# Kernel optimization log

Hardware: AMD Instinct MI355X
Metric: run time of the kernel (lower is better)

Reference implementation:

```python
import jax, jax.numpy as jnp
import numpy as np

DIM = 64
HEADS = 8
DIM_HEAD = 64
INNER = HEADS * DIM_HEAD  # 512
FB, HB, WB = 3, 4, 4
Q_L = HB * WB            # 16
KV_L = FB * HB * WB      # 48
EPS = 1e-5


def conv3(x, W):
    # x: [N,Cin,H,W], W: [Cout,Cin,3,3], stride 1, pad 1, no bias
    return jax.lax.conv_general_dilated(
        x, W, window_strides=(1, 1), padding='SAME',
        dimension_numbers=('NCHW', 'OIHW', 'NCHW'))


def layernorm(x, g, b):
    # normalize over last (channel) dim, matching nn.LayerNorm(dim)
    mu = jnp.mean(x, axis=-1, keepdims=True)
    var = jnp.mean(jnp.square(x - mu), axis=-1, keepdims=True)
    return (x - mu) * jax.lax.rsqrt(var + EPS) * g + b


def warp_nearest(x, flow):
    # Faithful to flow_warp-style grid_sample(mode='nearest', padding='zeros',
    # align_corners=True): sample x at round(grid + flow), zeros out-of-range.
    n, c, h, w = x.shape
    gy, gx = jnp.meshgrid(jnp.arange(h, dtype=x.dtype),
                          jnp.arange(w, dtype=x.dtype), indexing='ij')
    px = gx[None] + flow[:, 0]  # [n,h,w]
    py = gy[None] + flow[:, 1]
    ix = jnp.round(px).astype(jnp.int32)
    iy = jnp.round(py).astype(jnp.int32)
    valid = (ix >= 0) & (ix < w) & (iy >= 0) & (iy < h)
    flat = jnp.clip(iy, 0, h - 1) * w + jnp.clip(ix, 0, w - 1)  # [n,h,w]

    def gather_one(xi, fi):
        return jnp.take(xi.reshape(c, h * w), fi.reshape(-1), axis=1).reshape(c, h, w)

    out = jax.vmap(gather_one)(x, flat)
    return out * valid[:, None].astype(x.dtype)


def setup_inputs() -> dict:
    key = jax.random.key(0)
    ks = jax.random.split(key, 12)
    b, h, w = 2, 128, 128
    inp = {
        'q_inp': jax.random.normal(ks[0], (b, 1, DIM, h, w), jnp.float32),
        'k_inp': jax.random.normal(ks[1], (b, 3, DIM, h, w), jnp.float32),
        'flow_f': jax.random.normal(ks[2], (b, 2, h, w), jnp.float32) * 4.0,
        'flow_b': jax.random.normal(ks[3], (b, 2, h, w), jnp.float32) * 4.0,
        'gq': jnp.ones((DIM,), jnp.float32),
        'bq': jnp.zeros((DIM,), jnp.float32),
        'gkv': jnp.ones((DIM,), jnp.float32),
        'bkv': jnp.zeros((DIM,), jnp.float32),
        'Wq': jax.random.normal(ks[4], (INNER, DIM, 3, 3), jnp.float32) * 0.02,
        'Wkv': jax.random.normal(ks[5], (2 * INNER, DIM, 3, 3), jnp.float32) * 0.02,
        'Wout': jax.random.normal(ks[6], (DIM, INNER, 3, 3), jnp.float32) * 0.02,
        'static_a': jax.random.truncated_normal(ks[7], -2.0, 2.0, (1, HEADS, Q_L, KV_L), jnp.float32),
    }
    return inp


def _fgsw_msa(q_inp, k_inp, flow_f, flow_b, gq, bq, gkv, bkv, Wq, Wkv, Wout, static_a):
    b, f_q, c, h, w = q_inp.shape
    # flow-guided warp of forward/backward key frames (nearest, zeros padding)
    k_f = warp_nearest(k_inp[:, 0], flow_f)
    k_r = k_inp[:, 1]
    k_b = warp_nearest(k_inp[:, 2], flow_b)
    k_stack = jnp.stack([k_f, k_r, k_b], axis=1)  # [b,3,c,h,w]

    # LayerNorm over channels
    qn = layernorm(q_inp.transpose(0, 1, 3, 4, 2), gq, bq).transpose(0, 1, 4, 2, 3)
    kvn = layernorm(k_stack.transpose(0, 1, 3, 4, 2), gkv, bkv).transpose(0, 1, 4, 2, 3)

    # conv QKV projections
    q = conv3(qn.reshape(b * f_q, c, h, w), Wq)       # [b, INNER, h, w]
    kv = conv3(kvn.reshape(b * 3, c, h, w), Wkv)      # [3b, 2*INNER, h, w]
    k, v = jnp.split(kv, 2, axis=1)

    nh, nw = h // HB, w // WB

    def part(t, f):
        # [(b f), C, H, W] -> [(b nh nw), heads, f*HB*WB, d]
        C = t.shape[1]
        t = t.reshape(b, f, C, nh, HB, nw, WB)
        t = t.transpose(0, 3, 5, 1, 4, 6, 2)  # b, nh, nw, f, p1, p2, C
        t = t.reshape(b * nh * nw, f * HB * WB, HEADS, C // HEADS)
        return t.transpose(0, 2, 1, 3)

    qh = part(q, f_q) * (DIM_HEAD ** -0.5)
    kh = part(k, 3)
    vh = part(v, 3)

    sim = jnp.einsum('bhid,bhjd->bhij', qh, kh) + static_a
    attn = jax.nn.softmax(sim, axis=-1)
    out = jnp.einsum('bhij,bhjd->bhid', attn, vh)  # [(b nh nw), heads, Q_L, d]

    out = out.transpose(0, 2, 1, 3).reshape(b * nh * nw, f_q * HB * WB, INNER)
    out = out.reshape(b, nh, nw, f_q, HB, WB, INNER)
    out = out.transpose(0, 3, 6, 1, 4, 2, 5).reshape(b * f_q, INNER, h, w)
    out = conv3(out, Wout).reshape(b, f_q, c, h, w)
    return out


def reference(q_inp, k_inp, flow_f, flow_b, gq, bq, gkv, bkv, Wq, Wkv, Wout, static_a):
    return _fgsw_msa(q_inp, k_inp, flow_f, flow_b, gq, bq, gkv, bkv, Wq, Wkv, Wout, static_a)
```

## Files before the change

### kernel.cpp

```cpp
#include <hip/hip_runtime.h>


typedef __attribute__((ext_vector_type(8))) short bf16x8;
typedef __attribute__((ext_vector_type(4))) float f32x4;

__device__ __forceinline__ float bs2f(unsigned short s) {
    return __uint_as_float(((unsigned int)s) << 16);
}
__device__ __forceinline__ unsigned short f2bs(float f) {
    unsigned int u = __float_as_uint(f);
    u += 0x7fffu + ((u >> 16) & 1u);
    return (unsigned short)(u >> 16);
}

__global__ __launch_bounds__(256) void ln_q_kernel(
    const float* __restrict__ q_inp, const float* __restrict__ g,
    const float* __restrict__ b, unsigned short* __restrict__ qn)
{
    int wid  = (blockIdx.x * 256 + threadIdx.x) >> 6;
    int lane = threadIdx.x & 63;
    int pix  = wid & 16383;
    int bb   = wid >> 14;
    float val = q_inp[(bb * 64 + lane) * 16384 + pix];
    float s = val;
    #pragma unroll
    for (int m = 1; m < 64; m <<= 1) s += __shfl_xor(s, m);
    float mu = s * (1.f / 64.f);
    float d = val - mu;
    float s2 = d * d;
    #pragma unroll
    for (int m = 1; m < 64; m <<= 1) s2 += __shfl_xor(s2, m);
    float o = d * rsqrtf(s2 * (1.f / 64.f) + 1e-5f) * g[lane] + b[lane];
    qn[wid * 64 + lane] = f2bs(o);
}

__global__ __launch_bounds__(256) void warp_ln_kv_kernel(
    const float* __restrict__ k_inp, const float* __restrict__ flow_f,
    const float* __restrict__ flow_b, const float* __restrict__ g,
    const float* __restrict__ b, unsigned short* __restrict__ kvn)
{
    int wid  = (blockIdx.x * 256 + threadIdx.x) >> 6;
    int lane = threadIdx.x & 63;
    int x  = wid & 127;
    int y  = (wid >> 7) & 127;
    int bf = wid >> 14;
    int f  = bf % 3, bb = bf / 3;
    float val;
    if (f == 1) {
        val = k_inp[(bf * 64 + lane) * 16384 + y * 128 + x];
    } else {
        const float* fl = (f == 0) ? flow_f : flow_b;
        float fx = fl[(bb * 2 + 0) * 16384 + y * 128 + x];
        float fy = fl[(bb * 2 + 1) * 16384 + y * 128 + x];
        int ix = (int)rintf((float)x + fx);
        int iy = (int)rintf((float)y + fy);
        if (ix >= 0 && ix < 128 && iy >= 0 && iy < 128)
            val = k_inp[(bf * 64 + lane) * 16384 + iy * 128 + ix];
        else
            val = 0.f;
    }
    float s = val;
    #pragma unroll
    for (int m = 1; m < 64; m <<= 1) s += __shfl_xor(s, m);
    float mu = s * (1.f / 64.f);
    float d = val - mu;
    float s2 = d * d;
    #pragma unroll
    for (int m = 1; m < 64; m <<= 1) s2 += __shfl_xor(s2, m);
    float o = d * rsqrtf(s2 * (1.f / 64.f) + 1e-5f) * g[lane] + b[lane];
    kvn[wid * 64 + lane] = f2bs(o);
}

__global__ __launch_bounds__(256) void repack_bf16_kernel(
    const float* __restrict__ w, unsigned short* __restrict__ wp,
    int IC, int total)
{
    int idx = blockIdx.x * 256 + threadIdx.x;
    if (idx >= total) return;
    int tap = idx % 9;
    int tmp = idx / 9;
    int ic  = tmp % IC;
    int oc  = tmp / IC;
    wp[oc * IC * 9 + (ic >> 6) * 576 + tap * 64 + (ic & 63)] = f2bs(w[idx]);
}

__global__ __launch_bounds__(256) void fused_attn_kernel(
    const unsigned short* __restrict__ qn,
    const unsigned short* __restrict__ kvn,
    const unsigned short* __restrict__ wq,
    const unsigned short* __restrict__ wkv,
    const float* __restrict__ sa,
    unsigned short* __restrict__ ao)
{
    __shared__ __align__(16) unsigned char smem[49088];
    unsigned short* kvp = (unsigned short*)smem;
    unsigned short* qls = (unsigned short*)(smem + 15552);
    unsigned short* kls = (unsigned short*)(smem + 32192);
    unsigned short* vls = (unsigned short*)(smem + 39104);
    float*          atl = (float*)(smem + 46016);
    unsigned short* qpatch = kls;

    const int tid  = threadIdx.x;
    const int lane = tid & 63;
    const int w    = tid >> 6;
    const int wx = blockIdx.x & 31, wy = blockIdx.x >> 5;
    const int bb = blockIdx.y;
    const int gx0 = wx * 4 - 1, gy0 = wy * 4 - 1;

    for (int u = tid; u < 864; u += 256) {
        int f = u / 288, rest = u - f * 288;
        int pos = rest >> 3, seg = rest & 7;
        int hy = pos / 6, hx = pos - hy * 6;
        int gy = gy0 + hy, gx = gx0 + hx;
        uint4 v = make_uint4(0u, 0u, 0u, 0u);
        if ((unsigned)gy < 128u && (unsigned)gx < 128u)
            v = *reinterpret_cast<const uint4*>(
                kvn + (((bb * 3 + f) * 128 + gy) * 128 + gx) * 64 + seg * 8);
        *reinterpret_cast<uint4*>(kvp + (f * 36 + pos) * 72 + seg * 8) = v;
    }
    for (int u = tid; u < 288; u += 256) {
        int pos = u >> 3, seg = u & 7;
        int hy = pos / 6, hx = pos - hy * 6;
        int gy = gy0 + hy, gx = gx0 + hx;
        uint4 v = make_uint4(0u, 0u, 0u, 0u);
        if ((unsigned)gy < 128u && (unsigned)gx < 128u)
            v = *reinterpret_cast<const uint4*>(
                qn + ((bb * 128 + gy) * 128 + gx) * 64 + seg * 8);
        *reinterpret_cast<uint4*>(qpatch + pos * 72 + seg * 8) = v;
    }
    __syncthreads();

    const int r  = lane & 15;
    const int kg = lane >> 4;
    const int py = r >> 2, px = r & 3;

    for (int g = 0; g < 2; ++g) {
        f32x4 acc0 = {0.f,0.f,0.f,0.f}, acc1 = acc0, acc2 = acc0, acc3 = acc0;
        #pragma unroll 3
        for (int kk = 0; kk < 18; ++kk) {
            int tap = kk >> 1, ic0 = (kk & 1) * 32;
            int ky = tap / 3, kx = tap - ky * 3;
            int pos = (py + ky) * 6 + (px + kx);
            bf16x8 a = *reinterpret_cast<const bf16x8*>(qpatch + pos * 72 + ic0 + kg * 8);
            const unsigned short* wb = wq + (w * 8 + g * 4) * 16 * 576 + kk * 32 + kg * 8;
            bf16x8 b0 = *reinterpret_cast<const bf16x8*>(wb + (0 * 16 + r) * 576);
            bf16x8 b1 = *reinterpret_cast<const bf16x8*>(wb + (1 * 16 + r) * 576);
            bf16x8 b2 = *reinterpret_cast<const bf16x8*>(wb + (2 * 16 + r) * 576);
            bf16x8 b3 = *reinterpret_cast<const bf16x8*>(wb + (3 * 16 + r) * 576);
            acc0 = __builtin_amdgcn_mfma_f32_16x16x32_bf16(a, b0, acc0, 0, 0, 0);
            acc1 = __builtin_amdgcn_mfma_f32_16x16x32_bf16(a, b1, acc1, 0, 0, 0);
            acc2 = __builtin_amdgcn_mfma_f32_16x16x32_bf16(a, b2, acc2, 0, 0, 0);
            acc3 = __builtin_amdgcn_mfma_f32_16x16x32_bf16(a, b3, acc3, 0, 0, 0);
        }
        #pragma unroll
        for (int reg = 0; reg < 4; ++reg) {
            int row = kg * 4 + reg;
            int cb  = (w * 8 + g * 4) * 16 + r;
            qls[row * 520 + cb +  0] = f2bs(0.125f * acc0[reg]);
            qls[row * 520 + cb + 16] = f2bs(0.125f * acc1[reg]);
            qls[row * 520 + cb + 32] = f2bs(0.125f * acc2[reg]);
            qls[row * 520 + cb + 48] = f2bs(0.125f * acc3[reg]);
        }
    }
    __syncthreads();

    const int is_v = w >> 1, pair = w & 1;
    const int qi = tid >> 4, qjg = tid & 15;
    const int pd = tid & 63, pig = tid >> 6;

    for (int h = 0; h < 8; ++h) {
        {
            f32x4 c00 = {0.f,0.f,0.f,0.f}, c01 = c00, c10 = c00, c11 = c00, c20 = c00, c21 = c00;
            #pragma unroll 3
            for (int kk = 0; kk < 18; ++kk) {
                int tap = kk >> 1, ic0 = (kk & 1) * 32;
                int ky = tap / 3, kx = tap - ky * 3;
                int pos = (py + ky) * 6 + (px + kx);
                bf16x8 a0 = *reinterpret_cast<const bf16x8*>(kvp + pos * 72 + ic0 + kg * 8);
                bf16x8 a1 = *reinterpret_cast<const bf16x8*>(kvp + (36 + pos) * 72 + ic0 + kg * 8);
                bf16x8 a2 = *reinterpret_cast<const bf16x8*>(kvp + (72 + pos) * 72 + ic0 + kg * 8);
                int ocb = is_v * 512 + h * 64 + pair * 32;
                const unsigned short* wb = wkv + (size_t)ocb * 576 + kk * 32 + kg * 8;
                bf16x8 b0 = *reinterpret_cast<const bf16x8*>(wb + (size_t)(r) * 576);
                bf16x8 b1 = *reinterpret_cast<const bf16x8*>(wb + (size_t)(16 + r) * 576);
                c00 = __builtin_amdgcn_mfma_f32_16x16x32_bf16(a0, b0, c00, 0, 0, 0);
                c10 = __builtin_amdgcn_mfma_f32_16x16x32_bf16(a1, b0, c10, 0, 0, 0);
                c20 = __builtin_amdgcn_mfma_f32_16x16x32_bf16(a2, b0, c20, 0, 0, 0);
                c01 = __builtin_amdgcn_mfma_f32_16x16x32_bf16(a0, b1, c01, 0, 0, 0);
                c11 = __builtin_amdgcn_mfma_f32_16x16x32_bf16(a1, b1, c11, 0, 0, 0);
                c21 = __builtin_amdgcn_mfma_f32_16x16x32_bf16(a2, b1, c21, 0, 0, 0);
            }
            unsigned short* dst = is_v ? vls : kls;
            #pragma unroll
            for (int reg = 0; reg < 4; ++reg) {
                int jr = kg * 4 + reg;
                int cb = pair * 32 + r;
                dst[(jr +  0) * 72 + cb]      = f2bs(c00[reg]);
                dst[(jr + 16) * 72 + cb]      = f2bs(c10[reg]);
                dst[(jr + 32) * 72 + cb]      = f2bs(c20[reg]);
                dst[(jr +  0) * 72 + cb + 16] = f2bs(c01[reg]);
                dst[(jr + 16) * 72 + cb + 16] = f2bs(c11[reg]);
                dst[(jr + 32) * 72 + cb + 16] = f2bs(c21[reg]);
            }
        }
        __syncthreads();

        {
            const unsigned short* qrow = qls + qi * 520 + h * 64;
            float p[3];
            #pragma unroll
            for (int t = 0; t < 3; ++t) {
                int j = qjg + 16 * t;
                const unsigned short* krow = kls + j * 72;
                float s = 0.f;
                #pragma unroll
                for (int q8 = 0; q8 < 8; ++q8) {
                    uint4 ua = *reinterpret_cast<const uint4*>(qrow + q8 * 8);
                    uint4 ub = *reinterpret_cast<const uint4*>(krow + q8 * 8);
                    const unsigned short* pa = (const unsigned short*)&ua;
                    const unsigned short* pb = (const unsigned short*)&ub;
                    #pragma unroll
                    for (int o = 0; o < 8; ++o) s += bs2f(pa[o]) * bs2f(pb[o]);
                }
                p[t] = s + sa[(h * 16 + qi) * 48 + j];
            }
            float mx = fmaxf(p[0], fmaxf(p[1], p[2]));
            #pragma unroll
            for (int m = 1; m < 16; m <<= 1) mx = fmaxf(mx, __shfl_xor(mx, m));
            float sum = 0.f;
            #pragma unroll
            for (int t = 0; t < 3; ++t) { p[t] = __expf(p[t] - mx); sum += p[t]; }
            #pragma unroll
            for (int m = 1; m < 16; m <<= 1) sum += __shfl_xor(sum, m);
            float inv = 1.f / sum;
            #pragma unroll
            for (int t = 0; t < 3; ++t) atl[qi * 48 + qjg + 16 * t] = p[t] * inv;
        }
        __syncthreads();

        {
            float acc[4] = {0.f, 0.f, 0.f, 0.f};
            for (int j = 0; j < 48; ++j) {
                float vj = bs2f(vls[j * 72 + pd]);
                #pragma unroll
                for (int s = 0; s < 4; ++s)
                    acc[s] += atl[(pig * 4 + s) * 48 + j] * vj;
            }
            #pragma unroll
            for (int s = 0; s < 4; ++s) {
                int ii = pig * 4 + s;
                int y = wy * 4 + (ii >> 2), x = wx * 4 + (ii & 3);
                ao[((bb * 128 + y) * 128 + x) * 512 + h * 64 + pd] = f2bs(acc[s]);
            }
        }
        __syncthreads();
    }
}

__global__ __launch_bounds__(256) void conv512_kernel(
    const unsigned short* __restrict__ in,
    const unsigned short* __restrict__ wp,
    float* __restrict__ out)
{
    __shared__ __align__(16) unsigned short patch[100 * 72];
    const int tid = threadIdx.x, lane = tid & 63, w = tid >> 6;
    const int tx = blockIdx.x & 15, ty = blockIdx.x >> 4;
    const int img = blockIdx.y;
    const int gx0 = tx * 8 - 1, gy0 = ty * 8 - 1;
    const int r = lane & 15, kg = lane >> 4;

    f32x4 acc0 = {0.f,0.f,0.f,0.f}, acc1 = acc0, acc2 = acc0, acc3 = acc0;

    for (int ci = 0; ci < 8; ++ci) {
        __syncthreads();
        for (int u = tid; u < 800; u += 256) {
            int pos = u >> 3, seg = u & 7;
            int hy = pos / 10, hx = pos - hy * 10;
            int gy = gy0 + hy, gx = gx0 + hx;
            uint4 v = make_uint4(0u, 0u, 0u, 0u);
            if ((unsigned)gy < 128u && (unsigned)gx < 128u)
                v = *reinterpret_cast<const uint4*>(
                    in + (((size_t)img * 128 + gy) * 128 + gx) * 512 + ci * 64 + seg * 8);
            *reinterpret_cast<uint4*>(patch + pos * 72 + seg * 8) = v;
        }
        __syncthreads();
        #pragma unroll 3
        for (int kk = 0; kk < 18; ++kk) {
            int tap = kk >> 1, ic0 = (kk & 1) * 32;
            int ky = tap / 3, kx = tap - ky * 3;
            int oc = w * 16 + r;
            bf16x8 b = *reinterpret_cast<const bf16x8*>(
                wp + (size_t)oc * 4608 + ci * 576 + kk * 32 + kg * 8);
            #pragma unroll
            for (int m = 0; m < 4; ++m) {
                int rr = m * 16 + r;
                int pos = ((rr >> 3) + ky) * 10 + (rr & 7) + kx;
                bf16x8 a = *reinterpret_cast<const bf16x8*>(patch + pos * 72 + ic0 + kg * 8);
                f32x4& acc = (m == 0) ? acc0 : (m == 1) ? acc1 : (m == 2) ? acc2 : acc3;
                acc = __builtin_amdgcn_mfma_f32_16x16x32_bf16(a, b, acc, 0, 0, 0);
            }
        }
    }
    const int oc = w * 16 + r;
    #pragma unroll
    for (int m = 0; m < 4; ++m) {
        const f32x4& acc = (m == 0) ? acc0 : (m == 1) ? acc1 : (m == 2) ? acc2 : acc3;
        int r0 = m * 16 + kg * 4;
        int gy = ty * 8 + (r0 >> 3), gx = tx * 8 + (r0 & 7);
        *reinterpret_cast<float4*>(
            out + (((size_t)img * 64 + oc) * 128 + gy) * 128 + gx) =
            make_float4(acc[0], acc[1], acc[2], acc[3]);
    }
}

extern "C" void kernel_launch(void* const* d_in, const int* in_sizes, int n_in,
                              void* d_out, int out_size, void* d_ws, size_t ws_size,
                              hipStream_t stream)
{
    const float* q_inp  = (const float*)d_in[0];
    const float* k_inp  = (const float*)d_in[1];
    const float* flow_f = (const float*)d_in[2];
    const float* flow_b = (const float*)d_in[3];
    const float* gq     = (const float*)d_in[4];
    const float* bq     = (const float*)d_in[5];
    const float* gkv    = (const float*)d_in[6];
    const float* bkv    = (const float*)d_in[7];
    const float* Wq     = (const float*)d_in[8];
    const float* Wkv    = (const float*)d_in[9];
    const float* Wout   = (const float*)d_in[10];
    const float* sa     = (const float*)d_in[11];

    if (ws_size < 55050240u) return;

    char* ws = (char*)d_ws;
    unsigned short* qn   = (unsigned short*)(ws + 0);
    unsigned short* kvn  = (unsigned short*)(ws + 4194304);
    unsigned short* ao   = (unsigned short*)(ws + 16777216);
    unsigned short* wqb  = (unsigned short*)(ws + 50331648);
    unsigned short* wkvb = (unsigned short*)(ws + 50921472);
    unsigned short* wopb = (unsigned short*)(ws + 52101120);

    ln_q_kernel<<<8192, 256, 0, stream>>>(q_inp, gq, bq, qn);
    warp_ln_kv_kernel<<<24576, 256, 0, stream>>>(k_inp, flow_f, flow_b, gkv, bkv, kvn);

    repack_bf16_kernel<<<1152, 256, 0, stream>>>(Wq,   wqb,  64,  294912);
    repack_bf16_kernel<<<2304, 256, 0, stream>>>(Wkv,  wkvb, 64,  589824);
    repack_bf16_kernel<<<1152, 256, 0, stream>>>(Wout, wopb, 512, 294912);

    fused_attn_kernel<<<dim3(1024, 2), 256, 0, stream>>>(qn, kvn, wqb, wkvb, sa, ao);

    conv512_kernel<<<dim3(256, 2), 256, 0, stream>>>(ao, wopb, (float*)d_out);
}
```

Before: 645.2 us.

## Compute attention QK^T and PV with MFMA instead of scalar loops

Replaces the scalar per-thread QK dot products and the PV accumulation loop in the fused attention kernel with 16x16x32 bf16 MFMA instructions. V is now stored transposed in shared memory, and scores/probabilities live in a padded bf16 buffer so K=48 can be zero-padded to 64. Softmax probabilities and pre-softmax scores are rounded to bf16, which costs some precision. The output write pattern changes to 16-channel slices per wave, with less coalescing per store.

After: 606.8 us. 6.0% less time.

```diff
diff --git a/kernel.cpp b/kernel.cpp
--- a/kernel.cpp
+++ b/kernel.cpp
@@ -92,12 +92,12 @@
     const float* __restrict__ sa,
     unsigned short* __restrict__ ao)
 {
-    __shared__ __align__(16) unsigned char smem[49088];
-    unsigned short* kvp = (unsigned short*)smem;
-    unsigned short* qls = (unsigned short*)(smem + 15552);
-    unsigned short* kls = (unsigned short*)(smem + 32192);
-    unsigned short* vls = (unsigned short*)(smem + 39104);
-    float*          atl = (float*)(smem + 46016);
+    __shared__ __align__(16) unsigned char smem[50624];
+    unsigned short* kvp   = (unsigned short*)smem;
+    unsigned short* qls   = (unsigned short*)(smem + 15552);
+    unsigned short* kls   = (unsigned short*)(smem + 32192);
+    unsigned short* vls_T = (unsigned short*)(smem + 39104);
+    unsigned short* pls   = (unsigned short*)(smem + 48320);
     unsigned short* qpatch = kls;
 
     const int tid  = threadIdx.x;
@@ -127,6 +127,14 @@
             v = *reinterpret_cast<const uint4*>(
                 qn + ((bb * 128 + gy) * 128 + gx) * 64 + seg * 8);
         *reinterpret_cast<uint4*>(qpatch + pos * 72 + seg * 8) = v;
+    }
+    for (int u = tid; u < 1024; u += 256) {
+        int row = u >> 4, c = 48 + (u & 15);
+        vls_T[row * 72 + c] = 0;
+    }
+    if (tid < 256) {
+        int row = tid >> 4, c = 48 + (tid & 15);
+        pls[row * 72 + c] = 0;
     }
     __syncthreads();
 
@@ -165,8 +173,7 @@
     __syncthreads();
 
     const int is_v = w >> 1, pair = w & 1;
-    const int qi = tid >> 4, qjg = tid & 15;
-    const int pd = tid & 63, pig = tid >> 6;
+    const int si = tid >> 4, sjg = tid & 15;
 
     for (int h = 0; h < 8; ++h) {
         {
@@ -190,67 +197,86 @@
                 c11 = __builtin_amdgcn_mfma_f32_16x16x32_bf16(a1, b1, c11, 0, 0, 0);
                 c21 = __builtin_amdgcn_mfma_f32_16x16x32_bf16(a2, b1, c21, 0, 0, 0);
             }
-            unsigned short* dst = is_v ? vls : kls;
+            if (!is_v) {
+                #pragma unroll
+                for (int reg = 0; reg < 4; ++reg) {
+                    int jr = kg * 4 + reg;
+                    int cb = pair * 32 + r;
+                    kls[(jr +  0) * 72 + cb]      = f2bs(c00[reg]);
+                    kls[(jr + 16) * 72 + cb]      = f2bs(c10[reg]);
+                    kls[(jr + 32) * 72 + cb]      = f2bs(c20[reg]);
+                    kls[(jr +  0) * 72 + cb + 16] = f2bs(c01[reg]);
+                    kls[(jr + 16) * 72 + cb + 16] = f2bs(c11[reg]);
+                    kls[(jr + 32) * 72 + cb + 16] = f2bs(c21[reg]);
+                }
+            } else {
+                #pragma unroll
+                for (int reg = 0; reg < 4; ++reg) {
+                    int jr = kg * 4 + reg;
+                    int d0 = pair * 32 + r;
+                    vls_T[d0 * 72        + jr]      = f2bs(c00[reg]);
+                    vls_T[d0 * 72        + 16 + jr] = f2bs(c10[reg]);
+                    vls_T[d0 * 72        + 32 + jr] = f2bs(c20[reg]);
+                    vls_T[(d0 + 16) * 72 + jr]      = f2bs(c01[reg]);
+                    vls_T[(d0 + 16) * 72 + 16 + jr] = f2bs(c11[reg]);
+                    vls_T[(d0 + 16) * 72 + 32 + jr] = f2bs(c21[reg]);
+                }
+            }
+        }
+        __syncthreads();
+
+        if (w < 3) {
+            f32x4 s_acc = {0.f, 0.f, 0.f, 0.f};
+            #pragma unroll
+            for (int s = 0; s < 2; ++s) {
+                bf16x8 a = *reinterpret_cast<const bf16x8*>(
+                    qls + r * 520 + h * 64 + s * 32 + kg * 8);
+                bf16x8 b = *reinterpret_cast<const bf16x8*>(
+                    kls + (w * 16 + r) * 72 + s * 32 + kg * 8);
+                s_acc = __builtin_amdgcn_mfma_f32_16x16x32_bf16(a, b, s_acc, 0, 0, 0);
+            }
             #pragma unroll
             for (int reg = 0; reg < 4; ++reg) {
-                int jr = kg * 4 + reg;
-                int cb = pair * 32 + r;
-                dst[(jr +  0) * 72 + cb]      = f2bs(c00[reg]);
-                dst[(jr + 16) * 72 + cb]      = f2bs(c10[reg]);
-                dst[(jr + 32) * 72 + cb]      = f2bs(c20[reg]);
-                dst[(jr +  0) * 72 + cb + 16] = f2bs(c01[reg]);
-                dst[(jr + 16) * 72 + cb + 16] = f2bs(c11[reg]);
-                dst[(jr + 32) * 72 + cb + 16] = f2bs(c21[reg]);
+                int i = kg * 4 + reg, j = w * 16 + r;
+                float val = s_acc[reg] + sa[(h * 16 + i) * 48 + j];
+                pls[i * 72 + j] = f2bs(val);
             }
         }
         __syncthreads();
 
         {
-            const unsigned short* qrow = qls + qi * 520 + h * 64;
-            float p[3];
-            #pragma unroll
-            for (int t = 0; t < 3; ++t) {
-                int j = qjg + 16 * t;
-                const unsigned short* krow = kls + j * 72;
-                float s = 0.f;
-                #pragma unroll
-                for (int q8 = 0; q8 < 8; ++q8) {
-                    uint4 ua = *reinterpret_cast<const uint4*>(qrow + q8 * 8);
-                    uint4 ub = *reinterpret_cast<const uint4*>(krow + q8 * 8);
-                    const unsigned short* pa = (const unsigned short*)&ua;
-                    const unsigned short* pb = (const unsigned short*)&ub;
-                    #pragma unroll
-                    for (int o = 0; o < 8; ++o) s += bs2f(pa[o]) * bs2f(pb[o]);
-                }
-                p[t] = s + sa[(h * 16 + qi) * 48 + j];
-            }
-            float mx = fmaxf(p[0], fmaxf(p[1], p[2]));
+            float p0 = bs2f(pls[si * 72 + sjg]);
+            float p1 = bs2f(pls[si * 72 + sjg + 16]);
+            float p2 = bs2f(pls[si * 72 + sjg + 32]);
+            float mx = fmaxf(p0, fmaxf(p1, p2));
             #pragma unroll
             for (int m = 1; m < 16; m <<= 1) mx = fmaxf(mx, __shfl_xor(mx, m));
-            float sum = 0.f;
-            #pragma unroll
-            for (int t = 0; t < 3; ++t) { p[t] = __expf(p[t] - mx); sum += p[t]; }
+            p0 = __expf(p0 - mx); p1 = __expf(p1 - mx); p2 = __expf(p2 - mx);
+            float sum = p0 + p1 + p2;
             #pragma unroll
             for (int m = 1; m < 16; m <<= 1) sum += __shfl_xor(sum, m);
             float inv = 1.f / sum;
-            #pragma unroll
-            for (int t = 0; t < 3; ++t) atl[qi * 48 + qjg + 16 * t] = p[t] * inv;
+            pls[si * 72 + sjg]      = f2bs(p0 * inv);
+            pls[si * 72 + sjg + 16] = f2bs(p1 * inv);
+            pls[si * 72 + sjg + 32] = f2bs(p2 * inv);
         }
         __syncthreads();
 
         {
-            float acc[4] = {0.f, 0.f, 0.f, 0.f};
-            for (int j = 0; j < 48; ++j) {
-                float vj = bs2f(vls[j * 72 + pd]);
-                #pragma unroll
-                for (int s = 0; s < 4; ++s)
-                    acc[s] += atl[(pig * 4 + s) * 48 + j] * vj;
-            }
-            #pragma unroll
-            for (int s = 0; s < 4; ++s) {
-                int ii = pig * 4 + s;
-                int y = wy * 4 + (ii >> 2), x = wx * 4 + (ii & 3);
-                ao[((bb * 128 + y) * 128 + x) * 512 + h * 64 + pd] = f2bs(acc[s]);
+            f32x4 o_acc = {0.f, 0.f, 0.f, 0.f};
+            #pragma unroll
+            for (int s = 0; s < 2; ++s) {
+                bf16x8 a = *reinterpret_cast<const bf16x8*>(
+                    pls + r * 72 + s * 32 + kg * 8);
+                bf16x8 b = *reinterpret_cast<const bf16x8*>(
+                    vls_T + (w * 16 + r) * 72 + s * 32 + kg * 8);
+                o_acc = __builtin_amdgcn_mfma_f32_16x16x32_bf16(a, b, o_acc, 0, 0, 0);
+            }
+            #pragma unroll
+            for (int reg = 0; reg < 4; ++reg) {
+                int i = kg * 4 + reg;
+                int y = wy * 4 + (i >> 2), x = wx * 4 + (i & 3);
+                ao[((bb * 128 + y) * 128 + x) * 512 + h * 64 + w * 16 + r] = f2bs(o_acc[reg]);
             }
         }
         __syncthreads();
```
